# Performance work log

Hardware: AMD Instinct MI355X
Metric: run time of the kernel (lower is better)

The kernel has to match this reference:

```python
import jax, jax.numpy as jnp
import numpy as np

HEADS = 16
DIM_HEAD = 64
SCALE = DIM_HEAD ** -0.5


def setup_inputs() -> dict:
    key = jax.random.key(0)
    k1, k2, k3 = jax.random.split(key, 3)
    dim, inner = 1024, HEADS * DIM_HEAD
    b, n = 2, 2048
    x = jax.random.normal(k1, (b, n, dim), dtype=jnp.float32)
    w_qkv = jax.random.normal(k2, (dim, 3 * inner), dtype=jnp.float32) * (dim ** -0.5)
    w_out = jax.random.normal(k3, (inner, dim), dtype=jnp.float32) * (inner ** -0.5)
    b_out = jnp.zeros((dim,), dtype=jnp.float32)
    return {"x": x, "w_qkv": w_qkv, "w_out": w_out, "b_out": b_out}


def reference(x, w_qkv, w_out, b_out):
    b, n, _ = x.shape
    qkv = x @ w_qkv                                   # [b,n,3*inner]
    q, k, v = jnp.split(qkv, 3, axis=-1)
    def to_heads(t):
        return t.reshape(b, n, HEADS, DIM_HEAD).transpose(0, 2, 1, 3)  # [b,h,n,d]
    q, k, v = to_heads(q), to_heads(k), to_heads(v)
    dots = jnp.einsum('bhid,bhjd->bhij', q, k) * SCALE  # [b,h,n,n]
    attn = jax.nn.softmax(dots, axis=-1)
    out = jnp.einsum('bhij,bhjd->bhid', attn, v)        # [b,h,n,d]
    out = out.transpose(0, 2, 1, 3).reshape(b, n, HEADS * DIM_HEAD)
    return out @ w_out + b_out
```

## Files before the change

kernel.cpp:

```cpp
#include <hip/hip_runtime.h>
#include <hip/hip_bf16.h>

typedef unsigned short u16;
typedef unsigned int u32;
typedef __attribute__((ext_vector_type(8))) short short8;
typedef __attribute__((ext_vector_type(4))) float f32x4;
typedef __attribute__((ext_vector_type(16))) float f32x16;
typedef __attribute__((ext_vector_type(2))) u32 u32x2;

typedef __attribute__((address_space(1))) void as1_void;
typedef __attribute__((address_space(3))) void as3_void;

__device__ __forceinline__ u16 f2b(float x) {
    union { float f; u32 u; } c; c.f = x;
    u32 r = c.u + 0x7fffu + ((c.u >> 16) & 1u);
    return (u16)(r >> 16);
}
__device__ __forceinline__ float b2f(u16 x) {
    union { u32 u; float f; } c; c.u = ((u32)x) << 16;
    return c.f;
}
__device__ __forceinline__ u32 cvtpk(float lo, float hi) {
    u32 r;
    asm("v_cvt_pk_bf16_f32 %0, %1, %2" : "=v"(r) : "v"(lo), "v"(hi));
    return r;
}
__device__ __forceinline__ void gload16(const u16* g, u16* l) {
    __builtin_amdgcn_global_load_lds((as1_void*)(u16*)g, (as3_void*)l, 16, 0, 0);
}

__global__ __launch_bounds__(256) void convert_cvt(const float* __restrict__ in,
                                                   u16* __restrict__ out, int n8) {
    int i = blockIdx.x * 256 + threadIdx.x;
    if (i >= n8) return;
    const float4* p = (const float4*)(in + (size_t)i * 8);
    float4 a = p[0], b = p[1];
    short8 v;
    v[0]=(short)f2b(a.x); v[1]=(short)f2b(a.y); v[2]=(short)f2b(a.z); v[3]=(short)f2b(a.w);
    v[4]=(short)f2b(b.x); v[5]=(short)f2b(b.y); v[6]=(short)f2b(b.z); v[7]=(short)f2b(b.w);
    *(short8*)(out + (size_t)i * 8) = v;
}

__global__ __launch_bounds__(256) void transpose_cvt(const float* __restrict__ in,
                                                     u16* __restrict__ out, int R, int C) {
    __shared__ u16 tile[64][72];
    const int t = threadIdx.x;
    const int r0 = blockIdx.y * 64, c0 = blockIdx.x * 64;
    {
        const int rr = t >> 2;
        const int cq = (t & 3) * 16;
        const float* src = in + (size_t)(r0 + rr) * C + c0 + cq;
        #pragma unroll
        for (int j = 0; j < 4; j++) {
            float4 v = *(const float4*)(src + j * 4);
            tile[cq + j*4 + 0][rr] = f2b(v.x);
            tile[cq + j*4 + 1][rr] = f2b(v.y);
            tile[cq + j*4 + 2][rr] = f2b(v.z);
            tile[cq + j*4 + 3][rr] = f2b(v.w);
        }
    }
    __syncthreads();
    {
        const int cc = t >> 2;
        const int rq = (t & 3) * 16;
        u16* dst = out + (size_t)(c0 + cc) * R + r0 + rq;
        *(short8*)(dst)     = *(const short8*)&tile[cc][rq];
        *(short8*)(dst + 8) = *(const short8*)&tile[cc][rq + 8];
    }
}

template<bool QKV_MODE>
__global__ __launch_bounds__(256) void gemm128(const u16* __restrict__ A,
                                               const u16* __restrict__ Bt,
                                               void* __restrict__ Cp,
                                               u16* __restrict__ vt,
                                               const float* __restrict__ bias,
                                               int M, int Nn, int K) {
    __shared__ __align__(16) u16 a_lds[128 * 32];
    __shared__ __align__(16) u16 b_lds[128 * 32];
    const int tid = threadIdx.x;
    const int w = tid >> 6, l = tid & 63;
    const int l16 = l & 15, lg = l >> 4;
    const int m0 = blockIdx.y * 128, n0 = blockIdx.x * 128;
    const int wm = w >> 1, wn = w & 1;
    const int lr = l >> 2;
    const int scol = (l & 3) * 8;

    f32x4 acc[4][4];
    #pragma unroll
    for (int i = 0; i < 4; i++)
        #pragma unroll
        for (int j = 0; j < 4; j++) { f32x4 z = {0.f,0.f,0.f,0.f}; acc[i][j] = z; }

    const u16* Ap = A  + (size_t)m0 * K;
    const u16* Bp = Bt + (size_t)n0 * K;

    const int nk = K >> 5;
    for (int kt = 0; kt < nk; kt++) {
        const int kof = kt * 32;
        __syncthreads();
        #pragma unroll
        for (int j = 0; j < 2; j++) {
            const int r = w * 32 + j * 16;
            gload16(Ap + (size_t)(r + lr) * K + kof + scol, &a_lds[r * 32]);
            gload16(Bp + (size_t)(r + lr) * K + kof + scol, &b_lds[r * 32]);
        }
        asm volatile("s_waitcnt vmcnt(0)" ::: "memory");
        __syncthreads();
        short8 af[4], bf8[4];
        #pragma unroll
        for (int mb = 0; mb < 4; mb++)
            af[mb] = *(const short8*)&a_lds[(wm * 64 + mb * 16 + l16) * 32 + lg * 8];
        #pragma unroll
        for (int nb = 0; nb < 4; nb++)
            bf8[nb] = *(const short8*)&b_lds[(wn * 64 + nb * 16 + l16) * 32 + lg * 8];
        #pragma unroll
        for (int mb = 0; mb < 4; mb++)
            #pragma unroll
            for (int nb = 0; nb < 4; nb++)
                acc[mb][nb] = __builtin_amdgcn_mfma_f32_16x16x32_bf16(af[mb], bf8[nb], acc[mb][nb], 0, 0, 0);
    }

    #pragma unroll
    for (int mb = 0; mb < 4; mb++) {
        #pragma unroll
        for (int nb = 0; nb < 4; nb++) {
            const int col = n0 + wn * 64 + nb * 16 + l16;
            const int row0 = m0 + wm * 64 + mb * 16 + lg * 4;
            if constexpr (QKV_MODE) {
                if (col < 2048) {
                    #pragma unroll
                    for (int r = 0; r < 4; r++)
                        ((u16*)Cp)[(size_t)(row0 + r) * Nn + col] = f2b(acc[mb][nb][r]);
                } else {
                    const int hd = col - 2048;
                    const int hh = hd >> 6, d = hd & 63;
                    const int bi = row0 >> 11, n = row0 & 2047;
                    u32x2 pr;
                    pr.x = cvtpk(acc[mb][nb][0], acc[mb][nb][1]);
                    pr.y = cvtpk(acc[mb][nb][2], acc[mb][nb][3]);
                    *(u32x2*)(vt + ((size_t)((bi * 16 + hh) * 64 + d)) * 2048 + n) = pr;
                }
            } else {
                #pragma unroll
                for (int r = 0; r < 4; r++)
                    ((float*)Cp)[(size_t)(row0 + r) * Nn + col] = acc[mb][nb][r] + bias[col];
            }
        }
    }
}

__global__ __launch_bounds__(512, 2) void attn_kernel(const u16* __restrict__ qkv,
                                                      const u16* __restrict__ vt,
                                                      u16* __restrict__ out) {
    __shared__ __align__(16) u16 k_lds[8192];
    __shared__ __align__(16) u16 v_lds[8192];
    const int tid = threadIdx.x;
    const int w = tid >> 6, l = tid & 63;
    const int l31 = l & 31, hi = l >> 5;
    const int bb = blockIdx.z, h = blockIdx.y;
    const int q0 = blockIdx.x * 256 + w * 32;
    const int swzl = (l31 & 7) << 3;

    const u16* qp = qkv + (size_t)(bb * 2048 + q0 + l31) * 3072 + h * 64 + hi * 8;
    short8 qf[4];
    #pragma unroll
    for (int c4 = 0; c4 < 4; c4++) {
        short8 v = *(const short8*)(qp + c4 * 16);
        #pragma unroll
        for (int e = 0; e < 8; e++) v[e] = (short)f2b(b2f((u16)v[e]) * 0.125f);
        qf[c4] = v;
    }

    f32x16 o[2];
    #pragma unroll
    for (int d0 = 0; d0 < 2; d0++)
        #pragma unroll
        for (int e = 0; e < 16; e++) o[d0][e] = 0.f;
    float mrow = -1e30f, lsum = 0.f;

    const int srow = tid >> 3, scol = tid & 7;
    const int kd = srow * 64 + ((scol ^ (srow & 7)) * 8);
    const u16* ksrc = qkv + (size_t)(bb * 2048 + srow) * 3072 + 1024 + h * 64 + scol * 8;
    const u16* vsrc = vt + (size_t)((bb * 16 + h) * 64 + srow) * 2048 + scol * 8;

    short8 krg = *(const short8*)ksrc;
    short8 vrg = *(const short8*)vsrc;
    ksrc += 64 * 3072; vsrc += 64;
    *(short8*)&k_lds[kd] = krg;
    *(short8*)&v_lds[kd] = vrg;
    __syncthreads();

#define DO_TILE(CUR, NXT)                                                               \
  {                                                                                     \
     \
    krg = *(const short8*)ksrc; vrg = *(const short8*)vsrc;                             \
    ksrc += 64 * 3072; vsrc += 64;                                                      \
    f32x16 st[2];                                                                       \
    _Pragma("unroll") for (int tt = 0; tt < 2; tt++)                                    \
      _Pragma("unroll") for (int e = 0; e < 16; e++) st[tt][e] = 0.f;                   \
    _Pragma("unroll")                                                                   \
    for (int c4 = 0; c4 < 4; c4++) {                                                    \
      short8 kf0 = *(const short8*)&k_lds[(CUR) + (l31)*64      + ((c4*16 + hi*8) ^ swzl)]; \
      short8 kf1 = *(const short8*)&k_lds[(CUR) + (32 + l31)*64 + ((c4*16 + hi*8) ^ swzl)]; \
      st[0] = __builtin_amdgcn_mfma_f32_32x32x16_bf16(kf0, qf[c4], st[0], 0, 0, 0);     \
      st[1] = __builtin_amdgcn_mfma_f32_32x32x16_bf16(kf1, qf[c4], st[1], 0, 0, 0);     \
    }                                                                                   \
    float pmax = st[0][0];                                                              \
    _Pragma("unroll") for (int e = 1; e < 16; e++) pmax = fmaxf(pmax, st[0][e]);        \
    _Pragma("unroll") for (int e = 0; e < 16; e++) pmax = fmaxf(pmax, st[1][e]);        \
    const float rowm = fmaxf(pmax, __shfl_xor(pmax, 32));                               \
    if (__any(rowm > mrow + 5.5451774f)) {              \
      const float mnew  = fmaxf(mrow, rowm);                                            \
      const float alpha = __expf(mrow - mnew);                                          \
      lsum *= alpha;                                                                    \
      _Pragma("unroll") for (int d0 = 0; d0 < 2; d0++)                                  \
        _Pragma("unroll") for (int e = 0; e < 16; e++) o[d0][e] *= alpha;               \
      mrow = mnew;                                                                      \
    }                                                                                   \
    _Pragma("unroll") for (int tt = 0; tt < 2; tt++)                                    \
      _Pragma("unroll") for (int e = 0; e < 16; e++) st[tt][e] = __expf(st[tt][e] - mrow); \
    float psum = 0.f;                                                                   \
    _Pragma("unroll") for (int tt = 0; tt < 2; tt++)                                    \
      _Pragma("unroll") for (int e = 0; e < 16; e++) psum += st[tt][e];                 \
    lsum += psum + __shfl_xor(psum, 32);                                                \
    short8 pb[4];                                                                       \
    _Pragma("unroll")                                                                   \
    for (int tt = 0; tt < 2; tt++) {                                                    \
      _Pragma("unroll")                                                                 \
      for (int g = 0; g < 2; g++) {                                                     \
         \
        u32 w0 = cvtpk(st[tt][8*g + 0], st[tt][8*g + 1]);                               \
        u32 w1 = cvtpk(st[tt][8*g + 2], st[tt][8*g + 3]);                               \
        u32 w2 = cvtpk(st[tt][8*g + 4], st[tt][8*g + 5]);                               \
        u32 w3 = cvtpk(st[tt][8*g + 6], st[tt][8*g + 7]);                               \
        u32 w0x = (u32)__shfl_xor((int)w0, 32);                                         \
        u32 w1x = (u32)__shfl_xor((int)w1, 32);                                         \
        u32 w2x = (u32)__shfl_xor((int)w2, 32);                                         \
        u32 w3x = (u32)__shfl_xor((int)w3, 32);                                         \
        union { u32 wd[4]; short8 s8; } uu;                                             \
        uu.wd[0] = hi ? w2x : w0;                                                       \
        uu.wd[1] = hi ? w3x : w1;                                                       \
        uu.wd[2] = hi ? w2  : w0x;                                                      \
        uu.wd[3] = hi ? w3  : w1x;                                                      \
        pb[2*tt + g] = uu.s8;                                                           \
      }                                                                                 \
    }                                                                                   \
    _Pragma("unroll")                                                                   \
    for (int ks = 0; ks < 4; ks++) {                                                    \
      short8 vf0 = *(const short8*)&v_lds[(CUR) + (l31)*64      + ((ks*16 + hi*8) ^ swzl)]; \
      short8 vf1 = *(const short8*)&v_lds[(CUR) + (32 + l31)*64 + ((ks*16 + hi*8) ^ swzl)]; \
      o[0] = __builtin_amdgcn_mfma_f32_32x32x16_bf16(vf0, pb[ks], o[0], 0, 0, 0);       \
      o[1] = __builtin_amdgcn_mfma_f32_32x32x16_bf16(vf1, pb[ks], o[1], 0, 0, 0);       \
    }                                                                                   \
    *(short8*)&k_lds[(NXT) + kd] = krg;                                                 \
    *(short8*)&v_lds[(NXT) + kd] = vrg;                                                 \
    __syncthreads();                                                                    \
  }

    for (int it = 0; it < 16; it++) {
        DO_TILE(0, 4096)
        DO_TILE(4096, 0)
    }
#undef DO_TILE

    const float invl = 1.0f / lsum;
    u16* op = out + (size_t)(bb * 2048 + q0 + l31) * 1024 + h * 64;
    #pragma unroll
    for (int d0 = 0; d0 < 2; d0++) {
        #pragma unroll
        for (int s = 0; s < 4; s++) {
            u32x2 pr;
            pr.x = cvtpk(o[d0][4*s + 0] * invl, o[d0][4*s + 1] * invl);
            pr.y = cvtpk(o[d0][4*s + 2] * invl, o[d0][4*s + 3] * invl);
            *(u32x2*)(op + d0 * 32 + s * 8 + hi * 4) = pr;
        }
    }
}

extern "C" void kernel_launch(void* const* d_in, const int* in_sizes, int n_in,
                              void* d_out, int out_size, void* d_ws, size_t ws_size,
                              hipStream_t stream) {
    const float* x     = (const float*)d_in[0];
    const float* w_qkv = (const float*)d_in[1];
    const float* w_out = (const float*)d_in[2];
    const float* b_out = (const float*)d_in[3];

    char* ws = (char*)d_ws;
    u16* xb    = (u16*)(ws);
    u16* wqkvT = (u16*)(ws + (size_t)( 8u << 20));
    u16* woutT = (u16*)(ws + (size_t)(14u << 20));
    u16* qkvb  = (u16*)(ws + (size_t)(16u << 20));
    u16* vtb   = (u16*)(ws + (size_t)(40u << 20));
    u16* aout  = (u16*)(ws + (size_t)(48u << 20));

    convert_cvt<<<2048, 256, 0, stream>>>(x, xb, 4096 * 1024 / 8);
    transpose_cvt<<<dim3(48, 16), 256, 0, stream>>>(w_qkv, wqkvT, 1024, 3072);
    transpose_cvt<<<dim3(16, 16), 256, 0, stream>>>(w_out, woutT, 1024, 1024);

    gemm128<true><<<dim3(24, 32), 256, 0, stream>>>(xb, wqkvT, qkvb, vtb, nullptr,
                                                    4096, 3072, 1024);
    attn_kernel<<<dim3(8, 16, 2), 512, 0, stream>>>(qkvb, vtb, aout);

    gemm128<false><<<dim3(8, 32), 256, 0, stream>>>(aout, woutT, d_out, nullptr, b_out,
                                                    4096, 1024, 1024);
}
```

Baseline: 138.0 us.

## Double-buffer GEMM LDS tiles to overlap global loads with MFMA

New measurement: 128.0 us. 1.08x faster.

```diff
diff --git a/kernel.cpp b/kernel.cpp
--- a/kernel.cpp
+++ b/kernel.cpp
@@ -27,6 +27,11 @@
 }
 __device__ __forceinline__ void gload16(const u16* g, u16* l) {
     __builtin_amdgcn_global_load_lds((as1_void*)(u16*)g, (as3_void*)l, 16, 0, 0);
+}
+__device__ __forceinline__ void barrier_raw() {
+    asm volatile("" ::: "memory");
+    __builtin_amdgcn_s_barrier();
+    asm volatile("" ::: "memory");
 }
 
 __global__ __launch_bounds__(256) void convert_cvt(const float* __restrict__ in,
@@ -76,8 +81,8 @@
                                                u16* __restrict__ vt,
                                                const float* __restrict__ bias,
                                                int M, int Nn, int K) {
-    __shared__ __align__(16) u16 a_lds[128 * 32];
-    __shared__ __align__(16) u16 b_lds[128 * 32];
+    __shared__ __align__(16) u16 a_lds[2][128 * 32];
+    __shared__ __align__(16) u16 b_lds[2][128 * 32];
     const int tid = threadIdx.x;
     const int w = tid >> 6, l = tid & 63;
     const int l16 = l & 15, lg = l >> 4;
@@ -95,31 +100,45 @@
     const u16* Ap = A  + (size_t)m0 * K;
     const u16* Bp = Bt + (size_t)n0 * K;
 
+#define STAGE(BUF, KOF)                                                              \
+    _Pragma("unroll")                                                                \
+    for (int j = 0; j < 2; j++) {                                                    \
+        const int r = w * 32 + j * 16;                                               \
+        gload16(Ap + (size_t)(r + lr) * K + (KOF) + scol, &a_lds[(BUF)][r * 32]);    \
+        gload16(Bp + (size_t)(r + lr) * K + (KOF) + scol, &b_lds[(BUF)][r * 32]);    \
+    }
+
     const int nk = K >> 5;
+    STAGE(0, 0)
+    int cur = 0;
     for (int kt = 0; kt < nk; kt++) {
-        const int kof = kt * 32;
-        __syncthreads();
-        #pragma unroll
-        for (int j = 0; j < 2; j++) {
-            const int r = w * 32 + j * 16;
-            gload16(Ap + (size_t)(r + lr) * K + kof + scol, &a_lds[r * 32]);
-            gload16(Bp + (size_t)(r + lr) * K + kof + scol, &b_lds[r * 32]);
+        if (kt + 1 < nk) {
+            STAGE(cur ^ 1, (kt + 1) << 5)
+            __builtin_amdgcn_sched_barrier(0);
+            asm volatile("s_waitcnt vmcnt(4)" ::: "memory");
+            __builtin_amdgcn_sched_barrier(0);
+        } else {
+            __builtin_amdgcn_sched_barrier(0);
+            asm volatile("s_waitcnt vmcnt(0)" ::: "memory");
+            __builtin_amdgcn_sched_barrier(0);
         }
-        asm volatile("s_waitcnt vmcnt(0)" ::: "memory");
-        __syncthreads();
+        barrier_raw();
         short8 af[4], bf8[4];
         #pragma unroll
         for (int mb = 0; mb < 4; mb++)
-            af[mb] = *(const short8*)&a_lds[(wm * 64 + mb * 16 + l16) * 32 + lg * 8];
+            af[mb] = *(const short8*)&a_lds[cur][(wm * 64 + mb * 16 + l16) * 32 + lg * 8];
         #pragma unroll
         for (int nb = 0; nb < 4; nb++)
-            bf8[nb] = *(const short8*)&b_lds[(wn * 64 + nb * 16 + l16) * 32 + lg * 8];
+            bf8[nb] = *(const short8*)&b_lds[cur][(wn * 64 + nb * 16 + l16) * 32 + lg * 8];
         #pragma unroll
         for (int mb = 0; mb < 4; mb++)
             #pragma unroll
             for (int nb = 0; nb < 4; nb++)
                 acc[mb][nb] = __builtin_amdgcn_mfma_f32_16x16x32_bf16(af[mb], bf8[nb], acc[mb][nb], 0, 0, 0);
-    }
+        barrier_raw();
+        cur ^= 1;
+    }
+#undef STAGE
 
     #pragma unroll
     for (int mb = 0; mb < 4; mb++) {
```
